# Performance work log

Measured on AMD Instinct MI355X. Metric: run time of the kernel, lower is better.

Reference implementation:

```python
import jax, jax.numpy as jnp
import numpy as np

N_EMBED = 2048
NUM_EXPERTS = 64
TOP_K = 8
B, S = 4, 4096


def setup_inputs() -> dict:
    key = jax.random.key(0)
    k_x, k_n, k_w1, k_b1, k_w2, k_b2 = jax.random.split(key, 6)
    bound = 1.0 / np.sqrt(N_EMBED)  # torch nn.Linear default init range
    return {
        "x": jax.random.normal(k_x, (B, S, N_EMBED), dtype=jnp.float32),
        "noise": jax.random.normal(k_n, (B, S, NUM_EXPERTS), dtype=jnp.float32),
        "W1": jax.random.uniform(k_w1, (N_EMBED, NUM_EXPERTS), jnp.float32, -bound, bound),
        "b1": jax.random.uniform(k_b1, (NUM_EXPERTS,), jnp.float32, -bound, bound),
        "W2": jax.random.uniform(k_w2, (N_EMBED, NUM_EXPERTS), jnp.float32, -bound, bound),
        "b2": jax.random.uniform(k_b2, (NUM_EXPERTS,), jnp.float32, -bound, bound),
    }


def reference(x, noise, W1, b1, W2, b2):
    # logits = lin1(x); noise_scale = softplus(lin2(x))
    logits = jnp.einsum("bsd,de->bse", x, W1) + b1          # [B,S,E]
    scale = jax.nn.softplus(jnp.einsum("bsd,de->bse", x, W2) + b2)
    mixed = logits + noise * scale                            # [B,S,E]
    full = jax.nn.softmax(mixed, axis=-1)

    topk_vals, topk_idx = jax.lax.top_k(mixed, TOP_K)         # [B,S,K]

    # scatter topk values into a -inf background, then softmax (masked softmax)
    E = mixed.shape[-1]
    flat_mixed = mixed.reshape(-1, E)
    flat_idx = topk_idx.reshape(-1, TOP_K)
    flat_vals = topk_vals.reshape(-1, TOP_K)
    rows = jnp.arange(flat_mixed.shape[0])[:, None]
    sparse = jnp.full_like(flat_mixed, -jnp.inf).at[rows, flat_idx].set(flat_vals)
    sparse_sm = jax.nn.softmax(sparse, axis=-1).reshape(mixed.shape)

    return sparse_sm, topk_idx, full
```

## Files before the change

### kernel.cpp

```cpp
#include <hip/hip_runtime.h>
#include <math.h>


typedef _Float16 f16x8 __attribute__((ext_vector_type(8)));
typedef _Float16 f16x4 __attribute__((ext_vector_type(4)));
typedef float f32x4 __attribute__((ext_vector_type(4)));

constexpr int ND = 2048, NE = 64, NK = 8, NTOK = 16384;
constexpr int KC   = 32;
constexpr int NCHT = ND / KC;
constexpr int KS   = 2;
constexpr int CPS  = NCHT / KS;
constexpr int MTOK = 32;
constexpr int XROW = 40;
constexpr int XPLANE = MTOK * XROW;
constexpr int XBUF   = 2 * XPLANE;

__global__ void prep_w(const float* __restrict__ W1, const float* __restrict__ W2,
                       _Float16* __restrict__ wt3) {
    const int g    = blockIdx.x * 256 + threadIdx.x;
    const int cg   = g >> 9;
    const int rem  = g & 511;
    const int t    = rem >> 6;
    const int lane = rem & 63;
    const int col  = lane & 15, q = lane >> 4;
    const int n    = t * 16 + col;
    const float* W = (t < 4) ? W1 : W2;
    const int cn   = n & 63;
    _Float16 h[8], l[8];
    #pragma unroll
    for (int j = 0; j < 8; ++j) {
        const float v = W[(size_t)(cg * 32 + q * 8 + j) * 64 + cn];
        const _Float16 hh = (_Float16)v;
        h[j] = hh;
        l[j] = (_Float16)((v - (float)hh) * 2048.0f);
    }
    *(f16x8*)&wt3[((size_t)(cg * 2 + 0) * 8 + t) * 512 + lane * 8] = *(f16x8*)h;
    *(f16x8*)&wt3[((size_t)(cg * 2 + 1) * 8 + t) * 512 + lane * 8] = *(f16x8*)l;
}

__global__ __launch_bounds__(256, 4)
void router_main(const float* __restrict__ x, const _Float16* __restrict__ wt3,
                 float* __restrict__ zpart) {
    __shared__ _Float16 xlds[2 * XBUF];
    const int tid  = threadIdx.x;
    const int lane = tid & 63;
    const int wu   = __builtin_amdgcn_readfirstlane(tid >> 6);
    const int col  = lane & 15, q = lane >> 4;
    const int mg   = blockIdx.x >> 1;
    const int ks   = blockIdx.x & 1;
    const long tok0 = (long)mg * MTOK;
    const int c0   = ks * CPS;
    const int ta   = 2 * wu, tb = 2 * wu + 1;

    const int ltok = tid >> 3;
    const int lsub = tid & 7;
    const float* xbase = x + (tok0 + ltok) * (size_t)ND + (size_t)c0 * KC + lsub * 4;

    f32x4 a0[2][2], a1[2][2];
    #pragma unroll
    for (int m = 0; m < 2; ++m)
        #pragma unroll
        for (int i = 0; i < 2; ++i)
            #pragma unroll
            for (int r = 0; r < 4; ++r) { a0[m][i][r] = 0.f; a1[m][i][r] = 0.f; }

    float4 xv = *(const float4*)xbase;

    for (int c = 0; c < CPS; ++c) {
        _Float16* xb = &xlds[(c & 1) * XBUF];

        {
            const _Float16 h0 = (_Float16)xv.x, h1 = (_Float16)xv.y,
                           h2 = (_Float16)xv.z, h3 = (_Float16)xv.w;
            const f16x4 hv = {h0, h1, h2, h3};
            const f16x4 lv = { (_Float16)((xv.x - (float)h0) * 2048.0f),
                               (_Float16)((xv.y - (float)h1) * 2048.0f),
                               (_Float16)((xv.z - (float)h2) * 2048.0f),
                               (_Float16)((xv.w - (float)h3) * 2048.0f) };
            *(f16x4*)&xb[ltok * XROW + lsub * 4]          = hv;
            *(f16x4*)&xb[XPLANE + ltok * XROW + lsub * 4] = lv;
        }
        __syncthreads();

        const size_t fb = (size_t)(c0 + c) * 2 * 8 * 512 + (size_t)lane * 8;
        const f16x8 bha = *(const f16x8*)&wt3[fb + ta * 512];
        const f16x8 bhb = *(const f16x8*)&wt3[fb + tb * 512];
        const f16x8 bla = *(const f16x8*)&wt3[fb + 8 * 512 + ta * 512];
        const f16x8 blb = *(const f16x8*)&wt3[fb + 8 * 512 + tb * 512];

        if (c + 1 < CPS) xv = *(const float4*)(xbase + (c + 1) * KC);

        #pragma unroll
        for (int mt = 0; mt < 2; ++mt) {
            const f16x8 ah = *(const f16x8*)&xb[(mt * 16 + col) * XROW + q * 8];
            const f16x8 al = *(const f16x8*)&xb[XPLANE + (mt * 16 + col) * XROW + q * 8];
            a0[mt][0] = __builtin_amdgcn_mfma_f32_16x16x32_f16(ah, bha, a0[mt][0], 0, 0, 0);
            a0[mt][1] = __builtin_amdgcn_mfma_f32_16x16x32_f16(ah, bhb, a0[mt][1], 0, 0, 0);
            a1[mt][0] = __builtin_amdgcn_mfma_f32_16x16x32_f16(ah, bla, a1[mt][0], 0, 0, 0);
            a1[mt][1] = __builtin_amdgcn_mfma_f32_16x16x32_f16(ah, blb, a1[mt][1], 0, 0, 0);
            a1[mt][0] = __builtin_amdgcn_mfma_f32_16x16x32_f16(al, bha, a1[mt][0], 0, 0, 0);
            a1[mt][1] = __builtin_amdgcn_mfma_f32_16x16x32_f16(al, bhb, a1[mt][1], 0, 0, 0);
        }
        __syncthreads();
    }

    float* zp = zpart + (size_t)ks * NTOK * 128;
    #pragma unroll
    for (int mt = 0; mt < 2; ++mt)
        #pragma unroll
        for (int i = 0; i < 2; ++i) {
            const int n = (2 * wu + i) * 16 + col;
            #pragma unroll
            for (int r = 0; r < 4; ++r) {
                const long token = tok0 + mt * 16 + q * 4 + r;
                zp[(size_t)token * 128 + n] = a0[mt][i][r] + a1[mt][i][r] * 4.8828125e-4f;
            }
        }
}

__global__ __launch_bounds__(256, 4)
void router_epi(const float* __restrict__ zpart, const float* __restrict__ noise,
                const float* __restrict__ b1, const float* __restrict__ b2,
                float* __restrict__ out_sparse, float* __restrict__ out_idx,
                float* __restrict__ out_full) {
    const int lane = threadIdx.x & 63;
    const int wu   = threadIdx.x >> 6;
    const float b1v = b1[lane];
    const float b2v = b2[lane];

    for (int tt = 0; tt < 4; ++tt) {
        const long tok = (long)blockIdx.x * 16 + wu * 4 + tt;
        const size_t r0 = (size_t)tok * 128;
        const size_t s1 = (size_t)NTOK * 128;
        const double z1d = (double)zpart[r0 + lane]      + (double)zpart[s1 + r0 + lane];
        const double z2d = (double)zpart[r0 + 64 + lane] + (double)zpart[s1 + r0 + 64 + lane];
        const float z1 = (float)z1d + b1v;
        const float z2 = (float)z2d + b2v;
        const float sc = (float)log1p(exp((double)z2));
        const float nz = noise[tok * NE + lane];
        const float mixed = z1 + nz * sc;

        float vmax = mixed;
        for (int off = 32; off; off >>= 1) vmax = fmaxf(vmax, __shfl_xor(vmax, off));
        const float e = expf(mixed - vmax);
        float denom = e;
        for (int off = 32; off; off >>= 1) denom += __shfl_xor(denom, off);
        const float fullv = e / denom;

        float cur = mixed;
        int   sel = 0;
        float myidxf = 0.0f;
        #pragma unroll
        for (int r = 0; r < NK; ++r) {
            float bv = cur; int bi = lane;
            for (int off = 32; off; off >>= 1) {
                const float ov = __shfl_xor(bv, off);
                const int   oi = __shfl_xor(bi, off);
                if (ov > bv || (ov == bv && oi < bi)) { bv = ov; bi = oi; }
            }
            if (lane == r)  myidxf = (float)bi;
            if (lane == bi) { sel = 1; cur = -INFINITY; }
        }

        const float es = sel ? e : 0.0f;
        float dsum = es;
        for (int off = 32; off; off >>= 1) dsum += __shfl_xor(dsum, off);
        const float sparsev = sel ? (e / dsum) : 0.0f;

        out_full[tok * NE + lane]   = fullv;
        out_sparse[tok * NE + lane] = sparsev;
        if (lane < NK) out_idx[tok * NK + lane] = myidxf;
    }
}

extern "C" void kernel_launch(void* const* d_in, const int* in_sizes, int n_in,
                              void* d_out, int out_size, void* d_ws, size_t ws_size,
                              hipStream_t stream) {
    const float* x     = (const float*)d_in[0];
    const float* noise = (const float*)d_in[1];
    const float* W1    = (const float*)d_in[2];
    const float* b1    = (const float*)d_in[3];
    const float* W2    = (const float*)d_in[4];
    const float* b2    = (const float*)d_in[5];

    float* out_sparse = (float*)d_out;
    float* out_idx    = out_sparse + (size_t)NTOK * NE;
    float* out_full   = out_idx + (size_t)NTOK * NK;

    _Float16* wt3 = (_Float16*)d_ws;
    float* zpart  = (float*)((char*)d_ws + ((size_t)1 << 20));

    prep_w<<<128, 256, 0, stream>>>(W1, W2, wt3);
    router_main<<<NTOK / MTOK * KS, 256, 0, stream>>>(x, wt3, zpart);
    router_epi<<<NTOK / 16, 256, 0, stream>>>(zpart, noise, b1, b2,
                                              out_sparse, out_idx, out_full);
}
```

Baseline: 256.6 us.

## Fuse GEMM and routing epilogue into one kernel, load x directly to registers

Merges the matmul kernel and the routing epilogue into a single kernel. Each block now processes all K chunks for its 32 tokens and stages the combined logits in LDS instead of writing partial sums to global memory. x is loaded straight from global into registers in MFMA fragment layout, with a one-chunk register prefetch, so the LDS staging and per-chunk barriers go away. The trade-offs are half as many blocks (no K-split), lower occupancy from launch bounds of 2, and less coalesced x loads, since each lane reads 32-byte pieces across rows.

```diff
diff --git a/kernel.cpp b/kernel.cpp
--- a/kernel.cpp
+++ b/kernel.cpp
@@ -3,7 +3,6 @@
 
 
 typedef _Float16 f16x8 __attribute__((ext_vector_type(8)));
-typedef _Float16 f16x4 __attribute__((ext_vector_type(4)));
 typedef float f32x4 __attribute__((ext_vector_type(4)));
 
 constexpr int ND = 2048, NE = 64, NK = 8, NTOK = 16384;
@@ -12,9 +11,7 @@
 constexpr int KS   = 2;
 constexpr int CPS  = NCHT / KS;
 constexpr int MTOK = 32;
-constexpr int XROW = 40;
-constexpr int XPLANE = MTOK * XROW;
-constexpr int XBUF   = 2 * XPLANE;
+constexpr int ZROW = 132;
 
 __global__ void prep_w(const float* __restrict__ W1, const float* __restrict__ W2,
                        _Float16* __restrict__ wt3) {
@@ -39,104 +36,131 @@
     *(f16x8*)&wt3[((size_t)(cg * 2 + 1) * 8 + t) * 512 + lane * 8] = *(f16x8*)l;
 }
 
-__global__ __launch_bounds__(256, 4)
-void router_main(const float* __restrict__ x, const _Float16* __restrict__ wt3,
-                 float* __restrict__ zpart) {
-    __shared__ _Float16 xlds[2 * XBUF];
+__device__ __forceinline__ void split8(const float4 a, const float4 b,
+                                       f16x8& hh, f16x8& ll) {
+    const _Float16 h0 = (_Float16)a.x, h1 = (_Float16)a.y,
+                   h2 = (_Float16)a.z, h3 = (_Float16)a.w;
+    const _Float16 h4 = (_Float16)b.x, h5 = (_Float16)b.y,
+                   h6 = (_Float16)b.z, h7 = (_Float16)b.w;
+    hh = (f16x8){h0, h1, h2, h3, h4, h5, h6, h7};
+    ll = (f16x8){(_Float16)((a.x - (float)h0) * 2048.0f),
+                 (_Float16)((a.y - (float)h1) * 2048.0f),
+                 (_Float16)((a.z - (float)h2) * 2048.0f),
+                 (_Float16)((a.w - (float)h3) * 2048.0f),
+                 (_Float16)((b.x - (float)h4) * 2048.0f),
+                 (_Float16)((b.y - (float)h5) * 2048.0f),
+                 (_Float16)((b.z - (float)h6) * 2048.0f),
+                 (_Float16)((b.w - (float)h7) * 2048.0f)};
+}
+
+__global__ __launch_bounds__(256, 2)
+void router_fused(const float* __restrict__ x, const _Float16* __restrict__ wt3,
+                  const float* __restrict__ noise,
+                  const float* __restrict__ b1, const float* __restrict__ b2,
+                  float* __restrict__ out_sparse, float* __restrict__ out_idx,
+                  float* __restrict__ out_full) {
+    __shared__ float zs[MTOK * ZROW];
     const int tid  = threadIdx.x;
     const int lane = tid & 63;
     const int wu   = __builtin_amdgcn_readfirstlane(tid >> 6);
     const int col  = lane & 15, q = lane >> 4;
-    const int mg   = blockIdx.x >> 1;
-    const int ks   = blockIdx.x & 1;
-    const long tok0 = (long)mg * MTOK;
-    const int c0   = ks * CPS;
-    const int ta   = 2 * wu, tb = 2 * wu + 1;
-
-    const int ltok = tid >> 3;
-    const int lsub = tid & 7;
-    const float* xbase = x + (tok0 + ltok) * (size_t)ND + (size_t)c0 * KC + lsub * 4;
+    const long tok0 = (long)blockIdx.x * MTOK;
+    const int ta = 2 * wu, tb = 2 * wu + 1;
+
+    const float* xr0 = x + (tok0 + col)      * (size_t)ND + q * 8;
+    const float* xr1 = x + (tok0 + 16 + col) * (size_t)ND + q * 8;
+    const _Float16* wl = wt3 + (size_t)lane * 8;
 
     f32x4 a0[2][2], a1[2][2];
+    f32x4 zk0[2][2];
+
+    auto zero_acc = [&]() {
+        #pragma unroll
+        for (int m = 0; m < 2; ++m)
+            #pragma unroll
+            for (int i = 0; i < 2; ++i)
+                #pragma unroll
+                for (int r = 0; r < 4; ++r) { a0[m][i][r] = 0.f; a1[m][i][r] = 0.f; }
+    };
+
+    auto run_seg = [&](const int cbeg) {
+        float4 x0a = *(const float4*)(xr0 + (size_t)cbeg * KC);
+        float4 x0b = *(const float4*)(xr0 + (size_t)cbeg * KC + 4);
+        float4 x1a = *(const float4*)(xr1 + (size_t)cbeg * KC);
+        float4 x1b = *(const float4*)(xr1 + (size_t)cbeg * KC + 4);
+        const _Float16* w0 = wl + (size_t)cbeg * 8192;
+        f16x8 bha = *(const f16x8*)(w0 + ta * 512);
+        f16x8 bhb = *(const f16x8*)(w0 + tb * 512);
+        f16x8 bla = *(const f16x8*)(w0 + 4096 + ta * 512);
+        f16x8 blb = *(const f16x8*)(w0 + 4096 + tb * 512);
+
+        auto body = [&]() {
+            f16x8 ah0, al0, ah1, al1;
+            split8(x0a, x0b, ah0, al0);
+            split8(x1a, x1b, ah1, al1);
+            a0[0][0] = __builtin_amdgcn_mfma_f32_16x16x32_f16(ah0, bha, a0[0][0], 0, 0, 0);
+            a0[0][1] = __builtin_amdgcn_mfma_f32_16x16x32_f16(ah0, bhb, a0[0][1], 0, 0, 0);
+            a1[0][0] = __builtin_amdgcn_mfma_f32_16x16x32_f16(ah0, bla, a1[0][0], 0, 0, 0);
+            a1[0][1] = __builtin_amdgcn_mfma_f32_16x16x32_f16(ah0, blb, a1[0][1], 0, 0, 0);
+            a1[0][0] = __builtin_amdgcn_mfma_f32_16x16x32_f16(al0, bha, a1[0][0], 0, 0, 0);
+            a1[0][1] = __builtin_amdgcn_mfma_f32_16x16x32_f16(al0, bhb, a1[0][1], 0, 0, 0);
+            a0[1][0] = __builtin_amdgcn_mfma_f32_16x16x32_f16(ah1, bha, a0[1][0], 0, 0, 0);
+            a0[1][1] = __builtin_amdgcn_mfma_f32_16x16x32_f16(ah1, bhb, a0[1][1], 0, 0, 0);
+            a1[1][0] = __builtin_amdgcn_mfma_f32_16x16x32_f16(ah1, bla, a1[1][0], 0, 0, 0);
+            a1[1][1] = __builtin_amdgcn_mfma_f32_16x16x32_f16(ah1, blb, a1[1][1], 0, 0, 0);
+            a1[1][0] = __builtin_amdgcn_mfma_f32_16x16x32_f16(al1, bha, a1[1][0], 0, 0, 0);
+            a1[1][1] = __builtin_amdgcn_mfma_f32_16x16x32_f16(al1, bhb, a1[1][1], 0, 0, 0);
+        };
+
+        for (int c = cbeg; c < cbeg + CPS - 1; ++c) {
+            const float4 y0a = *(const float4*)(xr0 + (size_t)(c + 1) * KC);
+            const float4 y0b = *(const float4*)(xr0 + (size_t)(c + 1) * KC + 4);
+            const float4 y1a = *(const float4*)(xr1 + (size_t)(c + 1) * KC);
+            const float4 y1b = *(const float4*)(xr1 + (size_t)(c + 1) * KC + 4);
+            const _Float16* wn = wl + (size_t)(c + 1) * 8192;
+            const f16x8 cha = *(const f16x8*)(wn + ta * 512);
+            const f16x8 chb = *(const f16x8*)(wn + tb * 512);
+            const f16x8 cla = *(const f16x8*)(wn + 4096 + ta * 512);
+            const f16x8 clb = *(const f16x8*)(wn + 4096 + tb * 512);
+            body();
+            x0a = y0a; x0b = y0b; x1a = y1a; x1b = y1b;
+            bha = cha; bhb = chb; bla = cla; blb = clb;
+        }
+        body();
+    };
+
+    zero_acc();
+    run_seg(0);
     #pragma unroll
     for (int m = 0; m < 2; ++m)
         #pragma unroll
         for (int i = 0; i < 2; ++i)
-            #pragma unroll
-            for (int r = 0; r < 4; ++r) { a0[m][i][r] = 0.f; a1[m][i][r] = 0.f; }
-
-    float4 xv = *(const float4*)xbase;
-
-    for (int c = 0; c < CPS; ++c) {
-        _Float16* xb = &xlds[(c & 1) * XBUF];
-
-        {
-            const _Float16 h0 = (_Float16)xv.x, h1 = (_Float16)xv.y,
-                           h2 = (_Float16)xv.z, h3 = (_Float16)xv.w;
-            const f16x4 hv = {h0, h1, h2, h3};
-            const f16x4 lv = { (_Float16)((xv.x - (float)h0) * 2048.0f),
-                               (_Float16)((xv.y - (float)h1) * 2048.0f),
-                               (_Float16)((xv.z - (float)h2) * 2048.0f),
-                               (_Float16)((xv.w - (float)h3) * 2048.0f) };
-            *(f16x4*)&xb[ltok * XROW + lsub * 4]          = hv;
-            *(f16x4*)&xb[XPLANE + ltok * XROW + lsub * 4] = lv;
-        }
-        __syncthreads();
-
-        const size_t fb = (size_t)(c0 + c) * 2 * 8 * 512 + (size_t)lane * 8;
-        const f16x8 bha = *(const f16x8*)&wt3[fb + ta * 512];
-        const f16x8 bhb = *(const f16x8*)&wt3[fb + tb * 512];
-        const f16x8 bla = *(const f16x8*)&wt3[fb + 8 * 512 + ta * 512];
-        const f16x8 blb = *(const f16x8*)&wt3[fb + 8 * 512 + tb * 512];
-
-        if (c + 1 < CPS) xv = *(const float4*)(xbase + (c + 1) * KC);
-
-        #pragma unroll
-        for (int mt = 0; mt < 2; ++mt) {
-            const f16x8 ah = *(const f16x8*)&xb[(mt * 16 + col) * XROW + q * 8];
-            const f16x8 al = *(const f16x8*)&xb[XPLANE + (mt * 16 + col) * XROW + q * 8];
-            a0[mt][0] = __builtin_amdgcn_mfma_f32_16x16x32_f16(ah, bha, a0[mt][0], 0, 0, 0);
-            a0[mt][1] = __builtin_amdgcn_mfma_f32_16x16x32_f16(ah, bhb, a0[mt][1], 0, 0, 0);
-            a1[mt][0] = __builtin_amdgcn_mfma_f32_16x16x32_f16(ah, bla, a1[mt][0], 0, 0, 0);
-            a1[mt][1] = __builtin_amdgcn_mfma_f32_16x16x32_f16(ah, blb, a1[mt][1], 0, 0, 0);
-            a1[mt][0] = __builtin_amdgcn_mfma_f32_16x16x32_f16(al, bha, a1[mt][0], 0, 0, 0);
-            a1[mt][1] = __builtin_amdgcn_mfma_f32_16x16x32_f16(al, bhb, a1[mt][1], 0, 0, 0);
-        }
-        __syncthreads();
-    }
-
-    float* zp = zpart + (size_t)ks * NTOK * 128;
+            zk0[m][i] = a0[m][i] + a1[m][i] * 4.8828125e-4f;
+
+    zero_acc();
+    run_seg(CPS);
+
     #pragma unroll
-    for (int mt = 0; mt < 2; ++mt)
+    for (int m = 0; m < 2; ++m)
         #pragma unroll
         for (int i = 0; i < 2; ++i) {
-            const int n = (2 * wu + i) * 16 + col;
+            const int n = (ta + i) * 16 + col;
             #pragma unroll
             for (int r = 0; r < 4; ++r) {
-                const long token = tok0 + mt * 16 + q * 4 + r;
-                zp[(size_t)token * 128 + n] = a0[mt][i][r] + a1[mt][i][r] * 4.8828125e-4f;
+                const float zk1 = a0[m][i][r] + a1[m][i][r] * 4.8828125e-4f;
+                const float comb = (float)((double)zk0[m][i][r] + (double)zk1);
+                zs[(m * 16 + q * 4 + r) * ZROW + n] = comb;
             }
         }
-}
-
-__global__ __launch_bounds__(256, 4)
-void router_epi(const float* __restrict__ zpart, const float* __restrict__ noise,
-                const float* __restrict__ b1, const float* __restrict__ b2,
-                float* __restrict__ out_sparse, float* __restrict__ out_idx,
-                float* __restrict__ out_full) {
-    const int lane = threadIdx.x & 63;
-    const int wu   = threadIdx.x >> 6;
+    __syncthreads();
+
     const float b1v = b1[lane];
     const float b2v = b2[lane];
-
-    for (int tt = 0; tt < 4; ++tt) {
-        const long tok = (long)blockIdx.x * 16 + wu * 4 + tt;
-        const size_t r0 = (size_t)tok * 128;
-        const size_t s1 = (size_t)NTOK * 128;
-        const double z1d = (double)zpart[r0 + lane]      + (double)zpart[s1 + r0 + lane];
-        const double z2d = (double)zpart[r0 + 64 + lane] + (double)zpart[s1 + r0 + 64 + lane];
-        const float z1 = (float)z1d + b1v;
-        const float z2 = (float)z2d + b2v;
+    for (int tt = 0; tt < 8; ++tt) {
+        const int lt = wu * 8 + tt;
+        const long tok = tok0 + lt;
+        const float z1 = zs[lt * ZROW + lane] + b1v;
+        const float z2 = zs[lt * ZROW + 64 + lane] + b2v;
         const float sc = (float)log1p(exp((double)z2));
         const float nz = noise[tok * NE + lane];
         const float mixed = z1 + nz * sc;
@@ -189,10 +213,8 @@
     float* out_full   = out_idx + (size_t)NTOK * NK;
 
     _Float16* wt3 = (_Float16*)d_ws;
-    float* zpart  = (float*)((char*)d_ws + ((size_t)1 << 20));
 
     prep_w<<<128, 256, 0, stream>>>(W1, W2, wt3);
-    router_main<<<NTOK / MTOK * KS, 256, 0, stream>>>(x, wt3, zpart);
-    router_epi<<<NTOK / 16, 256, 0, stream>>>(zpart, noise, b1, b2,
-                                              out_sparse, out_idx, out_full);
-}
+    router_fused<<<NTOK / MTOK, 256, 0, stream>>>(x, wt3, noise, b1, b2,
+                                                  out_sparse, out_idx, out_full);
+}
```

After: 285.8 us. 1.11x slower.

## Fuse router GEMM and epilogue into one kernel, dropping split-K partials

Applied to the files above, without the earlier changes.

Merges the main MFMA kernel and the softmax/top-k epilogue into one kernel. Each block now covers the full K dimension for its 32 tokens, which removes the split-K partial buffer written to and re-read from global memory. The x tile is staged four chunks at a time in XOR-swizzled LDS with a software-prefetched double buffer. The two K-halves are still summed in double to keep the earlier rounding behaviour. In exchange the grid has half as many blocks and occupancy drops from 4 to 2 blocks per SM, which may reduce latency hiding for the x stream.

```diff
diff --git a/kernel.cpp b/kernel.cpp
--- a/kernel.cpp
+++ b/kernel.cpp
@@ -9,12 +9,12 @@
 constexpr int ND = 2048, NE = 64, NK = 8, NTOK = 16384;
 constexpr int KC   = 32;
 constexpr int NCHT = ND / KC;
-constexpr int KS   = 2;
-constexpr int CPS  = NCHT / KS;
+constexpr int CPSG = 4;
+constexpr int NSTG = NCHT / CPSG;
+constexpr int HSTG = NSTG / 2;
 constexpr int MTOK = 32;
-constexpr int XROW = 40;
-constexpr int XPLANE = MTOK * XROW;
-constexpr int XBUF   = 2 * XPLANE;
+constexpr int ZROW = 132;
+constexpr int STG_F16 = CPSG * MTOK * 64;
 
 __global__ void prep_w(const float* __restrict__ W1, const float* __restrict__ W2,
                        _Float16* __restrict__ wt3) {
@@ -39,25 +39,38 @@
     *(f16x8*)&wt3[((size_t)(cg * 2 + 1) * 8 + t) * 512 + lane * 8] = *(f16x8*)l;
 }
 
-__global__ __launch_bounds__(256, 4)
-void router_main(const float* __restrict__ x, const _Float16* __restrict__ wt3,
-                 float* __restrict__ zpart) {
-    __shared__ _Float16 xlds[2 * XBUF];
+__device__ __forceinline__ void split4(const float4 v, f16x4& hh, f16x4& ll) {
+    const _Float16 h0 = (_Float16)v.x, h1 = (_Float16)v.y,
+                   h2 = (_Float16)v.z, h3 = (_Float16)v.w;
+    hh = (f16x4){h0, h1, h2, h3};
+    ll = (f16x4){(_Float16)((v.x - (float)h0) * 2048.0f),
+                 (_Float16)((v.y - (float)h1) * 2048.0f),
+                 (_Float16)((v.z - (float)h2) * 2048.0f),
+                 (_Float16)((v.w - (float)h3) * 2048.0f)};
+}
+
+__global__ __launch_bounds__(256, 2)
+void router_fused(const float* __restrict__ x, const _Float16* __restrict__ wt3,
+                  const float* __restrict__ noise,
+                  const float* __restrict__ b1, const float* __restrict__ b2,
+                  float* __restrict__ out_sparse, float* __restrict__ out_idx,
+                  float* __restrict__ out_full) {
+    __shared__ __align__(16) _Float16 stage[2][STG_F16];
     const int tid  = threadIdx.x;
     const int lane = tid & 63;
     const int wu   = __builtin_amdgcn_readfirstlane(tid >> 6);
     const int col  = lane & 15, q = lane >> 4;
-    const int mg   = blockIdx.x >> 1;
-    const int ks   = blockIdx.x & 1;
-    const long tok0 = (long)mg * MTOK;
-    const int c0   = ks * CPS;
-    const int ta   = 2 * wu, tb = 2 * wu + 1;
-
-    const int ltok = tid >> 3;
-    const int lsub = tid & 7;
-    const float* xbase = x + (tok0 + ltok) * (size_t)ND + (size_t)c0 * KC + lsub * 4;
-
-    f32x4 a0[2][2], a1[2][2];
+    const long tok0 = (long)blockIdx.x * MTOK;
+    const int ta = 2 * wu, tb = 2 * wu + 1;
+
+    const int stok = tid >> 3, lsub = tid & 7;
+    const float* xs = x + (tok0 + stok) * (size_t)ND + lsub * 4;
+    const int wS = lsub >> 1, wh = lsub & 1;
+
+    const _Float16* wla = wt3 + (size_t)ta * 512 + (size_t)lane * 8;
+    const _Float16* wlb = wt3 + (size_t)tb * 512 + (size_t)lane * 8;
+
+    f32x4 a0[2][2], a1[2][2], zk0[2][2];
     #pragma unroll
     for (int m = 0; m < 2; ++m)
         #pragma unroll
@@ -65,78 +78,97 @@
             #pragma unroll
             for (int r = 0; r < 4; ++r) { a0[m][i][r] = 0.f; a1[m][i][r] = 0.f; }
 
-    float4 xv = *(const float4*)xbase;
-
-    for (int c = 0; c < CPS; ++c) {
-        _Float16* xb = &xlds[(c & 1) * XBUF];
-
-        {
-            const _Float16 h0 = (_Float16)xv.x, h1 = (_Float16)xv.y,
-                           h2 = (_Float16)xv.z, h3 = (_Float16)xv.w;
-            const f16x4 hv = {h0, h1, h2, h3};
-            const f16x4 lv = { (_Float16)((xv.x - (float)h0) * 2048.0f),
-                               (_Float16)((xv.y - (float)h1) * 2048.0f),
-                               (_Float16)((xv.z - (float)h2) * 2048.0f),
-                               (_Float16)((xv.w - (float)h3) * 2048.0f) };
-            *(f16x4*)&xb[ltok * XROW + lsub * 4]          = hv;
-            *(f16x4*)&xb[XPLANE + ltok * XROW + lsub * 4] = lv;
+    {
+        float4 cur[4];
+        #pragma unroll
+        for (int j = 0; j < 4; ++j) cur[j] = *(const float4*)(xs + (size_t)j * KC);
+        #pragma unroll
+        for (int j = 0; j < 4; ++j) {
+            f16x4 hv, lv; split4(cur[j], hv, lv);
+            const int idx = ((j * MTOK + stok) << 6)
+                          + (((wS ^ (stok & 7) ^ ((j & 1) << 2)) << 3) + (wh << 2));
+            *(f16x4*)&stage[0][idx]      = hv;
+            *(f16x4*)&stage[0][idx ^ 32] = lv;
+        }
+    }
+    __syncthreads();
+
+    for (int s = 0; s < NSTG; ++s) {
+        const _Float16* rb = stage[s & 1];
+        float4 nxt[4];
+        if (s + 1 < NSTG) {
+            #pragma unroll
+            for (int j = 0; j < 4; ++j)
+                nxt[j] = *(const float4*)(xs + (size_t)(s + 1) * 128 + (size_t)j * KC);
+        }
+        #pragma unroll
+        for (int cc = 0; cc < CPSG; ++cc) {
+            const size_t cb = (size_t)(s * CPSG + cc) * 8192;
+            const f16x8 bha = *(const f16x8*)(wla + cb);
+            const f16x8 bhb = *(const f16x8*)(wlb + cb);
+            const f16x8 blx = *(const f16x8*)(wla + cb + 4096);
+            const f16x8 bly = *(const f16x8*)(wlb + cb + 4096);
+            const int swz = (cc & 1) << 2;
+            #pragma unroll
+            for (int mt = 0; mt < 2; ++mt) {
+                const int ridx = ((cc * MTOK + mt * 16 + col) << 6)
+                               + ((q ^ (col & 7) ^ swz) << 3);
+                const f16x8 ah = *(const f16x8*)&rb[ridx];
+                const f16x8 al = *(const f16x8*)&rb[ridx ^ 32];
+                a0[mt][0] = __builtin_amdgcn_mfma_f32_16x16x32_f16(ah, bha, a0[mt][0], 0, 0, 0);
+                a0[mt][1] = __builtin_amdgcn_mfma_f32_16x16x32_f16(ah, bhb, a0[mt][1], 0, 0, 0);
+                a1[mt][0] = __builtin_amdgcn_mfma_f32_16x16x32_f16(ah, blx, a1[mt][0], 0, 0, 0);
+                a1[mt][1] = __builtin_amdgcn_mfma_f32_16x16x32_f16(ah, bly, a1[mt][1], 0, 0, 0);
+                a1[mt][0] = __builtin_amdgcn_mfma_f32_16x16x32_f16(al, bha, a1[mt][0], 0, 0, 0);
+                a1[mt][1] = __builtin_amdgcn_mfma_f32_16x16x32_f16(al, bhb, a1[mt][1], 0, 0, 0);
+            }
+        }
+        if (s == HSTG - 1) {
+            #pragma unroll
+            for (int m = 0; m < 2; ++m)
+                #pragma unroll
+                for (int i = 0; i < 2; ++i) {
+                    zk0[m][i] = a0[m][i] + a1[m][i] * 4.8828125e-4f;
+                    #pragma unroll
+                    for (int r = 0; r < 4; ++r) { a0[m][i][r] = 0.f; a1[m][i][r] = 0.f; }
+                }
+        }
+        if (s + 1 < NSTG) {
+            _Float16* wb = stage[(s + 1) & 1];
+            #pragma unroll
+            for (int j = 0; j < 4; ++j) {
+                f16x4 hv, lv; split4(nxt[j], hv, lv);
+                const int idx = ((j * MTOK + stok) << 6)
+                              + (((wS ^ (stok & 7) ^ ((j & 1) << 2)) << 3) + (wh << 2));
+                *(f16x4*)&wb[idx]      = hv;
+                *(f16x4*)&wb[idx ^ 32] = lv;
+            }
         }
         __syncthreads();
-
-        const size_t fb = (size_t)(c0 + c) * 2 * 8 * 512 + (size_t)lane * 8;
-        const f16x8 bha = *(const f16x8*)&wt3[fb + ta * 512];
-        const f16x8 bhb = *(const f16x8*)&wt3[fb + tb * 512];
-        const f16x8 bla = *(const f16x8*)&wt3[fb + 8 * 512 + ta * 512];
-        const f16x8 blb = *(const f16x8*)&wt3[fb + 8 * 512 + tb * 512];
-
-        if (c + 1 < CPS) xv = *(const float4*)(xbase + (c + 1) * KC);
-
-        #pragma unroll
-        for (int mt = 0; mt < 2; ++mt) {
-            const f16x8 ah = *(const f16x8*)&xb[(mt * 16 + col) * XROW + q * 8];
-            const f16x8 al = *(const f16x8*)&xb[XPLANE + (mt * 16 + col) * XROW + q * 8];
-            a0[mt][0] = __builtin_amdgcn_mfma_f32_16x16x32_f16(ah, bha, a0[mt][0], 0, 0, 0);
-            a0[mt][1] = __builtin_amdgcn_mfma_f32_16x16x32_f16(ah, bhb, a0[mt][1], 0, 0, 0);
-            a1[mt][0] = __builtin_amdgcn_mfma_f32_16x16x32_f16(ah, bla, a1[mt][0], 0, 0, 0);
-            a1[mt][1] = __builtin_amdgcn_mfma_f32_16x16x32_f16(ah, blb, a1[mt][1], 0, 0, 0);
-            a1[mt][0] = __builtin_amdgcn_mfma_f32_16x16x32_f16(al, bha, a1[mt][0], 0, 0, 0);
-            a1[mt][1] = __builtin_amdgcn_mfma_f32_16x16x32_f16(al, bhb, a1[mt][1], 0, 0, 0);
-        }
-        __syncthreads();
-    }
-
-    float* zp = zpart + (size_t)ks * NTOK * 128;
+    }
+
+    float* zs = (float*)&stage[0][0];
     #pragma unroll
-    for (int mt = 0; mt < 2; ++mt)
+    for (int m = 0; m < 2; ++m)
         #pragma unroll
         for (int i = 0; i < 2; ++i) {
-            const int n = (2 * wu + i) * 16 + col;
+            const int n = (ta + i) * 16 + col;
             #pragma unroll
             for (int r = 0; r < 4; ++r) {
-                const long token = tok0 + mt * 16 + q * 4 + r;
-                zp[(size_t)token * 128 + n] = a0[mt][i][r] + a1[mt][i][r] * 4.8828125e-4f;
-            }
-        }
-}
-
-__global__ __launch_bounds__(256, 4)
-void router_epi(const float* __restrict__ zpart, const float* __restrict__ noise,
-                const float* __restrict__ b1, const float* __restrict__ b2,
-                float* __restrict__ out_sparse, float* __restrict__ out_idx,
-                float* __restrict__ out_full) {
-    const int lane = threadIdx.x & 63;
-    const int wu   = threadIdx.x >> 6;
+                const float zk1 = a0[m][i][r] + a1[m][i][r] * 4.8828125e-4f;
+                const float comb = (float)((double)zk0[m][i][r] + (double)zk1);
+                zs[(m * 16 + q * 4 + r) * ZROW + n] = comb;
+            }
+        }
+    __syncthreads();
+
     const float b1v = b1[lane];
     const float b2v = b2[lane];
-
-    for (int tt = 0; tt < 4; ++tt) {
-        const long tok = (long)blockIdx.x * 16 + wu * 4 + tt;
-        const size_t r0 = (size_t)tok * 128;
-        const size_t s1 = (size_t)NTOK * 128;
-        const double z1d = (double)zpart[r0 + lane]      + (double)zpart[s1 + r0 + lane];
-        const double z2d = (double)zpart[r0 + 64 + lane] + (double)zpart[s1 + r0 + 64 + lane];
-        const float z1 = (float)z1d + b1v;
-        const float z2 = (float)z2d + b2v;
+    for (int tt = 0; tt < 8; ++tt) {
+        const int lt = wu * 8 + tt;
+        const long tok = tok0 + lt;
+        const float z1 = zs[lt * ZROW + lane] + b1v;
+        const float z2 = zs[lt * ZROW + 64 + lane] + b2v;
         const float sc = (float)log1p(exp((double)z2));
         const float nz = noise[tok * NE + lane];
         const float mixed = z1 + nz * sc;
@@ -189,10 +221,8 @@
     float* out_full   = out_idx + (size_t)NTOK * NK;
 
     _Float16* wt3 = (_Float16*)d_ws;
-    float* zpart  = (float*)((char*)d_ws + ((size_t)1 << 20));
 
     prep_w<<<128, 256, 0, stream>>>(W1, W2, wt3);
-    router_main<<<NTOK / MTOK * KS, 256, 0, stream>>>(x, wt3, zpart);
-    router_epi<<<NTOK / 16, 256, 0, stream>>>(zpart, noise, b1, b2,
-                                              out_sparse, out_idx, out_full);
-}
+    router_fused<<<NTOK / MTOK, 256, 0, stream>>>(x, wt3, noise, b1, b2,
+                                                  out_sparse, out_idx, out_full);
+}
```

After: 262.5 us. 2.3% more time.
